# Kernel tuning notes

Hardware: AMD Instinct MI355X
Metric: run time of the kernel (lower is better)

Reference implementation:

```python
import jax, jax.numpy as jnp
import numpy as np

B, K, D, LS, NL = 32, 64, 256, 128, 2


def _xavier(key, shape):
    # torch xavier_uniform for Linear weight [out, in]
    fan_out, fan_in = shape[-2], shape[-1]
    lim = float(np.sqrt(6.0 / (fan_in + fan_out)))
    return jax.random.uniform(key, shape, jnp.float32, -lim, lim)


def setup_inputs():
    key = jax.random.key(0)
    ks = jax.random.split(key, 32)
    inp = {
        "X": jax.random.normal(ks[0], (B, K, D), jnp.float32),
        # per-layer stacked params [NL, ...]
        "k_w": _xavier(ks[1], (NL, D, D)),
        "q_w": _xavier(ks[2], (NL, D, D)),
        "rv_w1": _xavier(ks[3], (NL, D, 2 * D)),
        "rv_b1": jnp.zeros((NL, D), jnp.float32),
        "rv_w2": _xavier(ks[4], (NL, D, D)),
        "rv_b2": jnp.zeros((NL, D), jnp.float32),
        "ln_g": jnp.ones((NL, D), jnp.float32),
        "ln_b": jnp.zeros((NL, D), jnp.float32),
        "mlp_w1": _xavier(ks[5], (NL, D, D)),
        "mlp_b1": jnp.zeros((NL, D), jnp.float32),
        "mlp_w2": _xavier(ks[6], (NL, D, D)),
        "mlp_b2": jnp.zeros((NL, D), jnp.float32),
        "proj_w": _xavier(ks[7], (LS, D)),
        "proj_b": jnp.zeros((LS,), jnp.float32),
        "mu_w": _xavier(ks[8], (LS, LS)),
        "mu_b": jnp.zeros((LS,), jnp.float32),
        "sp_w": _xavier(ks[9], (LS, LS)),
        "sp_b": jnp.zeros((LS,), jnp.float32),
    }
    return inp


def _gelu(x):
    return jax.nn.gelu(x, approximate=False)


def _layernorm(x, g, b, eps=1e-5):
    m = jnp.mean(x, axis=-1, keepdims=True)
    v = jnp.mean((x - m) ** 2, axis=-1, keepdims=True)
    return (x - m) / jnp.sqrt(v + eps) * g + b


def _block(x, kw, qw, rw1, rb1, rw2, rb2, lg, lb, mw1, mb1, mw2, mb2):
    scale = D ** (-0.5)
    x_orig = x
    # pairwise difference r[b,i,j,:] = x[b,i]-x[b,j]
    r = x[:, :, None, :] - x[:, None, :, :]                      # [B,K,K,D]
    xi = jnp.broadcast_to(x[:, :, None, :], (B, K, K, D))
    cat = jnp.concatenate([xi, r], axis=-1)                      # [B,K,K,2D]
    v = _gelu(jnp.einsum('bijc,dc->bijd', cat, rw1) + rb1)
    v = jnp.einsum('bijd,ed->bije', v, rw2) + rb2                # [B,K,K,D]
    k = jnp.einsum('bid,ed->bie', x, kw)
    q = jnp.einsum('bid,ed->bie', x, qw) * scale
    attn = jax.nn.softmax(jnp.einsum('bid,bjd->bij', q, k), axis=2)
    agg = jnp.einsum('bij,bijd->bid', attn, v)
    h = _layernorm(x_orig + agg, lg, lb)
    h = jnp.einsum('bid,ed->bie', _gelu(jnp.einsum('bid,ed->bie', h, mw1) + mb1), mw2) + mb2
    return x_orig + h


def reference(X, k_w, q_w, rv_w1, rv_b1, rv_w2, rv_b2, ln_g, ln_b,
              mlp_w1, mlp_b1, mlp_w2, mlp_b2, proj_w, proj_b,
              mu_w, mu_b, sp_w, sp_b):
    x = X
    for i in range(NL):
        x = _block(x, k_w[i], q_w[i], rv_w1[i], rv_b1[i], rv_w2[i], rv_b2[i],
                   ln_g[i], ln_b[i], mlp_w1[i], mlp_b1[i], mlp_w2[i], mlp_b2[i])
    s = jnp.sum(x, axis=1)                                        # [B,D]
    h = _gelu(s @ proj_w.T + proj_b)                              # [B,LS]
    mu = h @ mu_w.T + mu_b
    scale = jax.nn.softplus(h @ sp_w.T + sp_b)
    return (mu, scale)
```

## Files before the change

### kernel.cpp

```cpp
#include <hip/hip_runtime.h>
#include <hip/hip_bf16.h>


using bf16 = __hip_bfloat16;
typedef short bf16x8 __attribute__((ext_vector_type(8)));
typedef float f32x4 __attribute__((ext_vector_type(4)));

__device__ __forceinline__ float bfu(unsigned short u) { return __uint_as_float(((unsigned)u) << 16); }

__device__ __forceinline__ unsigned short bfr(float v) {
  unsigned u = __float_as_uint(v);
  u += 0x7FFFu + ((u >> 16) & 1u);
  return (unsigned short)(u >> 16);
}

__device__ __forceinline__ float gelu_e(float x) {
  return 0.5f * x * (1.0f + erff(x * 0.7071067811865475f));
}

__device__ __forceinline__ float load_f(const void* p, int i, int fl) {
  if (fl) return bfu(((const unsigned short*)p)[i]);
  return ((const float*)p)[i];
}

__device__ __forceinline__ int block_detect(const void* X) {
  __shared__ int bad_s;
  if (threadIdx.x == 0) bad_s = 0;
  __syncthreads();
  if (threadIdx.x < 256) {
    const float v = bfu(((const unsigned short*)X)[threadIdx.x]);
    if (!(fabsf(v) < 1e6f)) atomicOr(&bad_s, 1);
  }
  __syncthreads();
  return bad_s ? 0 : 1;
}

__device__ __forceinline__ void stage_split4(unsigned short (&aF)[2][4096], int row, int d0, float4 v) {
  ushort4 h, lo;
  h.x = bfr(v.x); h.y = bfr(v.y); h.z = bfr(v.z); h.w = bfr(v.w);
  lo.x = bfr(v.x - bfu(h.x)); lo.y = bfr(v.y - bfu(h.y));
  lo.z = bfr(v.z - bfu(h.z)); lo.w = bfr(v.w - bfu(h.w));
  const int kt = d0 >> 5, lane = row | (((d0 >> 3) & 3) << 4), j = d0 & 7;
  *(ushort4*)&aF[0][kt*512 + lane*8 + j] = h;
  *(ushort4*)&aF[1][kt*512 + lane*8 + j] = lo;
}

__global__ __launch_bounds__(256) void prep_kernel(
    const void* __restrict__ X, const void* __restrict__ kw, const void* __restrict__ qw,
    const void* __restrict__ rw1, const void* __restrict__ rw2, const void* __restrict__ mw1,
    const void* __restrict__ mw2, const void* __restrict__ pw, const void* __restrict__ muw,
    const void* __restrict__ spw,
    const void* __restrict__ rb1, const void* __restrict__ rb2, const void* __restrict__ lng,
    const void* __restrict__ lnb, const void* __restrict__ mb1, const void* __restrict__ mb2,
    const void* __restrict__ pb, const void* __restrict__ mub, const void* __restrict__ spb,
    unsigned short* __restrict__ wfb, unsigned short* __restrict__ w3b,
    float* __restrict__ wh, float* __restrict__ bc)
{
  __shared__ __align__(16) char psm[65536];
  const int fl = block_detect(X);
  const int t = threadIdx.x;
  int blk = blockIdx.x;

  if (blk < 16) {
    unsigned short* ls = (unsigned short*)psm;
    unsigned* lsu = (unsigned*)psm;
    const int l = blk >> 3, kt = blk & 7;
    if (fl) {
      #pragma unroll
      for (int s = 0; s < 4; ++s) {
        const unsigned* sp = (const unsigned*)((s == 0) ? kw : (s == 1) ? qw : rw1);
        const int rstr = (s < 2) ? 128 : 256;
        const int coff = ((s == 3) ? 128 : 0) + kt*16;
        for (int i = t; i < 4096; i += 256) {
          const int e = i >> 4, d2 = i & 15;
          lsu[s*4096 + i] = sp[(l*256 + e)*rstr + coff + d2];
        }
      }
    } else {
      #pragma unroll
      for (int s = 0; s < 4; ++s) {
        const float* sp = (const float*)((s == 0) ? kw : (s == 1) ? qw : rw1);
        const int rstr = (s < 2) ? 256 : 512;
        const int coff = ((s == 3) ? 256 : 0) + kt*32;
        for (int i = t; i < 4096; i += 256) {
          const int e = i >> 4, d2 = i & 15;
          const float f0 = sp[(l*256 + e)*rstr + coff + d2*2];
          const float f1 = sp[(l*256 + e)*rstr + coff + d2*2 + 1];
          lsu[s*4096 + i] = (unsigned)bfr(f0) | ((unsigned)bfr(f1) << 16);
        }
      }
    }
    __syncthreads();
    unsigned* outp = (unsigned*)wfb + (l*8 + kt)*16384;
    for (int f2 = t; f2 < 16384; f2 += 256) {
      const int j2 = f2 & 3, lane = (f2 >> 2) & 63, ntg = f2 >> 8;
      const int seg = ntg >> 4;
      const int e = (ntg & 15)*16 + (lane & 15);
      const int dl = ((lane >> 4) & 3)*8 + j2*2;
      unsigned short r0 = ls[seg*8192 + e*32 + dl];
      unsigned short r1 = ls[seg*8192 + e*32 + dl + 1];
      if (seg == 1) { r0 = bfr(bfu(r0)*0.0625f); r1 = bfr(bfu(r1)*0.0625f); }
      else if (seg == 2) {
        const unsigned short w0 = ls[3*8192 + e*32 + dl];
        const unsigned short w1 = ls[3*8192 + e*32 + dl + 1];
        r0 = bfr(bfu(r0) + bfu(w0)); r1 = bfr(bfu(r1) + bfu(w1));
      }
      outp[f2] = (unsigned)r0 | ((unsigned)r1 << 16);
    }
    return;
// ... 34 lines not shown
  if (blk < 24) {
    float* lsf = (float*)psm;
    if (blk < 8) {
      const int l0 = blk*16;
      if (fl) {
        const unsigned* sp = (const unsigned*)pw;
        for (int i = t; i < 2048; i += 256) {
          const int ll = i >> 7, d2 = i & 127;
          const unsigned u = sp[(l0 + ll)*128 + d2];
          lsf[ll*256 + d2*2]     = __uint_as_float(u << 16);
          lsf[ll*256 + d2*2 + 1] = __uint_as_float(u & 0xffff0000u);
        }
      } else {
        const float* sp = (const float*)pw;
        for (int i = t; i < 4096; i += 256) {
          const int ll = i >> 8, d = i & 255;
          lsf[ll*256 + d] = sp[(l0 + ll)*256 + d];
        }
      }
      __syncthreads();
      for (int i = t; i < 4096; i += 256) {
        const int d = i >> 4, ll = i & 15;
        wh[d*128 + l0 + ll] = lsf[ll*256 + d];
      }
    } else {
      const int grp2 = blk - 8;
      const int isSp = grp2 >> 3;
      const int l0 = (grp2 & 7)*16;
      const void* src = isSp ? spw : muw;
      const int off = isSp ? 49152 : 32768;
      if (fl) {
        const unsigned* sp = (const unsigned*)src;
        for (int i = t; i < 1024; i += 256) {
          const int ll = i >> 6, c2 = i & 63;
          const unsigned u = sp[(l0 + ll)*64 + c2];
          lsf[ll*128 + c2*2]     = __uint_as_float(u << 16);
          lsf[ll*128 + c2*2 + 1] = __uint_as_float(u & 0xffff0000u);
        }
      } else {
        const float* sp = (const float*)src;
        for (int i = t; i < 2048; i += 256) {
          const int ll = i >> 7, c = i & 127;
          lsf[ll*128 + c] = sp[(l0 + ll)*128 + c];
        }
      }
      __syncthreads();
      for (int i = t; i < 2048; i += 256) {
        const int c = i >> 4, ll = i & 15;
        wh[off + c*128 + l0 + ll] = lsf[ll*128 + c];
      }
    }
    return;
  }
  for (int i = t; i < 3456; i += 256) {
    const void* src; int off;
    if (i < 512)       { src = rb1; off = i; }
    else if (i < 1024) { src = rb2; off = i - 512; }
    else if (i < 1536) { src = lng; off = i - 1024; }
    else if (i < 2048) { src = lnb; off = i - 1536; }
    else if (i < 2560) { src = mb1; off = i - 2048; }
    else if (i < 3072) { src = mb2; off = i - 2560; }
    else if (i < 3200) { src = pb;  off = i - 3072; }
    else if (i < 3328) { src = mub; off = i - 3200; }
    else               { src = spb; off = i - 3328; }
    bc[i] = load_f(src, off, fl);
  }
}

template<bool SPLIT, int NTG>
__device__ __forceinline__ void k1_body(
    const unsigned short (&aF)[2][4096],
    const unsigned short* __restrict__ wfb, const float* __restrict__ bc,
    float* __restrict__ kq, float* __restrict__ Pf, unsigned* __restrict__ Qpk,
    int l, int row0, int ntg0, int t)
{
  const int w = t >> 6, l64 = t & 63;
  const int col = l64 & 15, quad = l64 >> 4;
  f32x4 acc[NTG];
  #pragma unroll
  for (int i = 0; i < NTG; ++i) acc[i] = (f32x4){0.f, 0.f, 0.f, 0.f};
  for (int kt = 0; kt < 8; ++kt) {
    const bf16x8 ah = *(const bf16x8*)&aF[0][kt*512 + l64*8];
    bf16x8 al;
    if (SPLIT) al = *(const bf16x8*)&aF[1][kt*512 + l64*8];
    #pragma unroll
    for (int i = 0; i < NTG; ++i) {
      const int ntg = ntg0 + w*NTG + i;
      const bf16x8 b = *(const bf16x8*)&wfb[((l*8 + kt)*64 + ntg)*512 + l64*8];
      acc[i] = __builtin_amdgcn_mfma_f32_16x16x32_bf16(ah, b, acc[i], 0, 0, 0);
      if (SPLIT) acc[i] = __builtin_amdgcn_mfma_f32_16x16x32_bf16(al, b, acc[i], 0, 0, 0);
    }
  }
  #pragma unroll
  for (int i = 0; i < NTG; ++i) {
    const int ntg = ntg0 + w*NTG + i;
    if (ntg < 32) {
      const int n = ntg*16 + col;
      #pragma unroll
      for (int r = 0; r < 4; ++r)
        kq[(size_t)(row0 + quad*4 + r)*512 + n] = acc[i][r];
    } else if (ntg < 48) {
      const int c = (ntg - 32)*16 + col;
      const float bias = bc[l*256 + c];
      #pragma unroll
      for (int r = 0; r < 4; ++r)
        Pf[(size_t)(row0 + quad*4 + r)*256 + c] = acc[i][r] + bias;
    } else {
      #pragma unroll
      for (int r = 0; r < 4; ++r) {
        const float v = acc[i][r];
        const float pv = __shfl_xor(v, 1, 64);
        if (!(col & 1)) {
          const unsigned uu = (unsigned)bfr(v) | ((unsigned)bfr(pv) << 16);
          Qpk[(size_t)(row0 + quad*4 + r)*128 + (ntg - 48)*8 + (col >> 1)] = uu;
        }
      }
    }
  }
}

__global__ __launch_bounds__(256) void k1l0(
    const void* __restrict__ X, const unsigned short* __restrict__ wfb,
    const float* __restrict__ bc, float* __restrict__ kq, float* __restrict__ Pf,
    unsigned* __restrict__ Qpk)
{
  const int fl = block_detect(X);
  __shared__ __align__(16) unsigned short aF[2][4096];
  const int t = threadIdx.x;
  const int mb = (int)blockIdx.x >> 2, nb4 = (int)blockIdx.x & 3;
  const int row0 = mb * 16, ntg0 = nb4 * 16;
  if (fl) {
    for (int i = t; i < 512; i += 256) {
      const int row = i >> 5, d0 = (i & 31) * 8;
      const uint4 u = *(const uint4*)((const unsigned*)X + (size_t)(row0 + row)*128 + (i & 31)*4);
      const int kt = d0 >> 5, lane = row | (((d0 >> 3) & 3) << 4);
      *(uint4*)&aF[0][kt*512 + lane*8] = u;
    }
  } else {
    for (int i = t; i < 1024; i += 256) {
      const int row = i >> 6, d0 = (i & 63) * 4;
      stage_split4(aF, row, d0, *(const float4*)((const float*)X + (size_t)(row0 + row)*256 + d0));
    }
  }
  __syncthreads();
  if (fl) k1_body<false, 4>(aF, wfb, bc, kq, Pf, Qpk, 0, row0, ntg0, t);
  else    k1_body<true,  4>(aF, wfb, bc, kq, Pf, Qpk, 0, row0, ntg0, t);
}

__global__ __launch_bounds__(256) void k23_attn(
    const float* __restrict__ kq, const float* __restrict__ Pf,
    const unsigned* __restrict__ Qpk, float* __restrict__ g)
{
  __shared__ float qs[2][256];
  __shared__ float scp[2][64];
  __shared__ float als[2][64];
  const int t = threadIdx.x;
  const int b = (int)blockIdx.x >> 5, ip = (int)blockIdx.x & 31;
  const int base = b << 6, i0 = ip * 2;
  for (int i = t; i < 512; i += 256)
    qs[i >> 8][i & 255] = kq[(size_t)(base + i0 + (i >> 8))*512 + 256 + (i & 255)];
  __syncthreads();
  {
    const int w = t >> 6, lane = t & 63;
    const int jl = lane & 15, part = lane >> 4;
    const int j = w*16 + jl;
    const float* krow = kq + (size_t)(base + j)*512 + part*64;
    const float* q0p = &qs[0][part*64];
    const float* q1p = &qs[1][part*64];
    float s0 = 0.f, s1 = 0.f;
    for (int dd = 0; dd < 64; dd += 4) {
      const float4 kv = *(const float4*)&krow[dd];
      const float4 q0 = *(const float4*)&q0p[dd];
      const float4 q1 = *(const float4*)&q1p[dd];
      s0 = fmaf(kv.x, q0.x, s0); s0 = fmaf(kv.y, q0.y, s0);
      s0 = fmaf(kv.z, q0.z, s0); s0 = fmaf(kv.w, q0.w, s0);
      s1 = fmaf(kv.x, q1.x, s1); s1 = fmaf(kv.y, q1.y, s1);
      s1 = fmaf(kv.z, q1.z, s1); s1 = fmaf(kv.w, q1.w, s1);
    }
    s0 += __shfl_xor(s0, 16, 64); s0 += __shfl_xor(s0, 32, 64);
    s1 += __shfl_xor(s1, 16, 64); s1 += __shfl_xor(s1, 32, 64);
    if (part == 0) { scp[0][j] = s0; scp[1][j] = s1; }
  }
  __syncthreads();
  if (t < 128) {
    const int row = t >> 6, j = t & 63;
    float s = scp[row][j];
    float m = s;
    #pragma unroll
    for (int off = 32; off; off >>= 1) m = fmaxf(m, __shfl_xor(m, off, 64));
    const float e = __expf(s - m);
    float ss = e;
    #pragma unroll
    for (int off = 32; off; off >>= 1) ss += __shfl_xor(ss, off, 64);
    als[row][j] = e / ss;
  }
  __syncthreads();
  const int rg = t >> 7, cp = t & 127;
  const int r = base + i0 + rg;
  const float2 P = *(const float2*)&Pf[(size_t)r*256 + cp*2];
  const float A0 = -1.702f * P.x, A1 = -1.702f * P.y;
  const float* ap = &als[rg][0];
  const unsigned* qp = Qpk + (size_t)base*128 + cp;
  float acc0 = 0.f, acc1 = 0.f;
  #pragma unroll 8
  for (int j = 0; j < 64; ++j) {
    const unsigned u = qp[j*128];
    const float wgt = ap[j];
    const float q0 = __uint_as_float(u << 16);
    const float q1 = __uint_as_float(u & 0xffff0000u);
    const float s0 = __builtin_amdgcn_rcpf(1.f + __expf(fmaf(1.702f, q0, A0)));
    const float s1 = __builtin_amdgcn_rcpf(1.f + __expf(fmaf(1.702f, q1, A1)));
    acc0 = fmaf(wgt * (P.x - q0), s0, acc0);
    acc1 = fmaf(wgt * (P.y - q1), s1, acc1);
  }
  *(float2*)&g[(size_t)r*256 + cp*2] = make_float2(acc0, acc1);
}

__device__ __forceinline__ void k4_gemm8(
    f32x4 acc[2], const unsigned short (&aF)[2][4096],
    const unsigned short* __restrict__ wg, int w, int l64)
{
  acc[0] = (f32x4){0.f, 0.f, 0.f, 0.f};
  acc[1] = (f32x4){0.f, 0.f, 0.f, 0.f};
  for (int kt = 0; kt < 8; ++kt) {
    const bf16x8 ah = *(const bf16x8*)&aF[0][kt*512 + l64*8];
    const bf16x8 al = *(const bf16x8*)&aF[1][kt*512 + l64*8];
    #pragma unroll
    for (int nt = 0; nt < 2; ++nt) {
      const bf16x8 b = *(const bf16x8*)&wg[((kt*16 + (w*2 + nt))*64 + l64)*8];
      acc[nt] = __builtin_amdgcn_mfma_f32_16x16x32_bf16(ah, b, acc[nt], 0, 0, 0);
      acc[nt] = __builtin_amdgcn_mfma_f32_16x16x32_bf16(al, b, acc[nt], 0, 0, 0);
    }
  }
}

template<bool ADAPT, bool TAIL, int NR>
__device__ __forceinline__ void k4_core(
    const float* __restrict__ g, const void* __restrict__ xin, int fl,
    float* __restrict__ xout, const unsigned short* __restrict__ wg,
    const float* __restrict__ bc, int l, int row0, int t, bool writeX,
    unsigned short (&aF)[2][4096], float* bufB, float (&mv)[16][2])
{
  const int w = t >> 6, l64 = t & 63;
  const int col = l64 & 15, quad = l64 >> 4;
  const float* rb2c = bc + 512  + l*256;
  const float* lngc = bc + 1024 + l*256;
  const float* lnbc = bc + 1536 + l*256;
  const float* mb1c = bc + 2048 + l*256;
  const float* mb2c = bc + 2560 + l*256;

  for (int i = t; i < NR*64; i += 512) {
    const int row = i >> 6, d0 = (i & 63) * 4;
    stage_split4(aF, row, d0, *(const float4*)&g[(size_t)(row0 + row)*256 + d0]);
  }
  if (ADAPT && fl) {
    for (int c = t; c < NR*128; c += 512) {
      const int row = c >> 7, dp = c & 127;
      const unsigned u = ((const unsigned*)xin)[(size_t)(row0 + row)*128 + dp];
      bufB[row*260 + dp*2]     = __uint_as_float(u << 16);
      bufB[row*260 + dp*2 + 1] = __uint_as_float(u & 0xffff0000u);
    }
  } else {
    for (int c = t; c < NR*64; c += 512) {
      const int row = c >> 6, d0 = (c & 63) * 4;
      *(float4*)&bufB[row*260 + d0] = *(const float4*)((const float*)xin + (size_t)(row0 + row)*256 + d0);
    }
  }
  __syncthreads();
  float xtr[2][4];
  #pragma unroll
  for (int nt = 0; nt < 2; ++nt) {
    const int cn = (w*2 + nt)*16 + col;
    #pragma unroll
    for (int r = 0; r < 4; ++r) xtr[nt][r] = bufB[(quad*4 + r)*260 + cn];
  }
  __syncthreads();

  f32x4 acc[2];
  k4_gemm8(acc, aF, wg, w, l64);
  #pragma unroll
  for (int nt = 0; nt < 2; ++nt) {
    const int cn = (w*2 + nt)*16 + col;
    #pragma unroll
    for (int r = 0; r < 4; ++r)
      bufB[(quad*4 + r)*260 + cn] = acc[nt][r] + rb2c[cn] + xtr[nt][r];
  }
  __syncthreads();
  {
    const int row = t >> 5, part = t & 31;
    if (row < NR) {
      float s = 0.f, s2 = 0.f;
      #pragma unroll
      for (int kk = 0; kk < 8; ++kk) {
        const float v = bufB[row*260 + part + kk*32];
        s += v; s2 = fmaf(v, v, s2);
      }
      #pragma unroll
      for (int off = 16; off; off >>= 1) {
        s  += __shfl_xor(s, off, 32);
        s2 += __shfl_xor(s2, off, 32);
      }
      if (part == 0) {
        const float mu = s * (1.f/256.f);
        mv[row][0] = mu;
        mv[row][1] = rsqrtf(fmaf(-mu, mu, s2 * (1.f/256.f)) + 1e-5f);
      }
// ... 5 lines not shown
    float4 v = *(const float4*)&bufB[row*260 + d0];
    const float m = mv[row][0], iv = mv[row][1];
    v.x = (v.x - m)*iv*lngc[d0]   + lnbc[d0];
    v.y = (v.y - m)*iv*lngc[d0+1] + lnbc[d0+1];
    v.z = (v.z - m)*iv*lngc[d0+2] + lnbc[d0+2];
    v.w = (v.w - m)*iv*lngc[d0+3] + lnbc[d0+3];
    stage_split4(aF, row, d0, v);
  }
  __syncthreads();
  k4_gemm8(acc, aF, wg + 65536, w, l64);
  #pragma unroll
  for (int nt = 0; nt < 2; ++nt) {
    const int cn = (w*2 + nt)*16 + col;
    #pragma unroll
    for (int r = 0; r < 4; ++r)
      if (quad*4 + r < NR)
        bufB[(quad*4 + r)*260 + cn] = gelu_e(acc[nt][r] + mb1c[cn]);
  }
  __syncthreads();
  for (int i = t; i < NR*64; i += 512) {
    const int row = i >> 6, d0 = (i & 63) * 4;
    stage_split4(aF, row, d0, *(const float4*)&bufB[row*260 + d0]);
  }
  __syncthreads();
  k4_gemm8(acc, aF, wg + 2*65536, w, l64);
  if (TAIL) {
    #pragma unroll
    for (int nt = 0; nt < 2; ++nt) {
      const int cn = (w*2 + nt)*16 + col;
      #pragma unroll
      for (int r = 0; r < 4; ++r)
        bufB[(quad*4 + r)*260 + cn] = acc[nt][r] + mb2c[cn] + xtr[nt][r];
    }
    __syncthreads();
    for (int i = t; i < NR*64; i += 512) {
      const int row = i >> 6, d0 = (i & 63) * 4;
      const float4 v = *(const float4*)&bufB[row*260 + d0];
      if (writeX) *(float4*)&xout[(size_t)(row0 + row)*256 + d0] = v;
      stage_split4(aF, row, d0, v);
    }
    __syncthreads();
  } else {
    #pragma unroll
    for (int nt = 0; nt < 2; ++nt) {
      const int cn = (w*2 + nt)*16 + col;
      #pragma unroll
      for (int r = 0; r < 4; ++r)
        if (quad*4 + r < NR)
          xout[(size_t)(row0 + quad*4 + r)*256 + cn] = acc[nt][r] + mb2c[cn] + xtr[nt][r];
    }
  }
}

__global__ __launch_bounds__(512) void k41_mix_kq(
    const float* __restrict__ g, const unsigned short* __restrict__ w3b,
    const unsigned short* __restrict__ wfb, const float* __restrict__ bc,
    const void* __restrict__ X, float* __restrict__ x,
    float* __restrict__ kq, float* __restrict__ Pf, unsigned* __restrict__ Qpk)
{
  const int fl = block_detect(X);
  __shared__ __align__(16) unsigned short aF[2][4096];
  __shared__ float bufB[16*260];
  __shared__ float mv[16][2];
  const int t = threadIdx.x;
  const int rb = (int)blockIdx.x >> 1, parity = (int)blockIdx.x & 1;
  const int row0 = rb * 16;
  k4_core<true, true, 16>(g, X, fl, x, w3b, bc, 0, row0, t, parity == 0, aF, bufB, mv);
  k1_body<true, 4>(aF, wfb, bc, kq, Pf, Qpk, 1, row0, parity*32, t);
}

__global__ __launch_bounds__(512) void k4_fin(
    const float* __restrict__ g, const unsigned short* __restrict__ w3b,
    const float* __restrict__ bc, float* __restrict__ x)
{
  __shared__ __align__(16) unsigned short aF[2][4096];
  __shared__ float bufB[16*260];
  __shared__ float mv[16][2];
  const int t = threadIdx.x;
  const int row0 = blockIdx.x * 8;
  k4_core<false, false, 8>(g, x, 0, x, w3b + 3*65536, bc, 1, row0, t, true, aF, bufB, mv);
}

__global__ __launch_bounds__(256) void k5_head(
    const float* __restrict__ x, const float* __restrict__ wh,
    const float* __restrict__ bc, const void* __restrict__ X,
    void* __restrict__ out)
{
  const int fl = block_detect(X);
  __shared__ float ss[256];
  __shared__ float hh[128];
  const int b = blockIdx.x, t = threadIdx.x;
  float s = 0.f;
  for (int i = 0; i < 64; ++i) s += x[(size_t)((b << 6) + i)*256 + t];
  ss[t] = s;
  __syncthreads();
  if (t < 128) {
    float acc = bc[3072 + t];
    const float* projT = wh;
    for (int d = 0; d < 256; ++d) acc = fmaf(ss[d], projT[d*128 + t], acc);
    hh[t] = gelu_e(acc);
  }
  __syncthreads();
  float v; int oidx;
  if (t < 128) {
    float acc = bc[3200 + t];
    const float* muT = wh + 32768;
    for (int c = 0; c < 128; ++c) acc = fmaf(hh[c], muT[c*128 + t], acc);
    v = acc; oidx = b*128 + t;
  } else {
    const int u = t - 128;
    float acc = bc[3328 + u];
    const float* spT = wh + 49152;
    for (int c = 0; c < 128; ++c) acc = fmaf(hh[c], spT[c*128 + u], acc);
    v = (acc > 20.f) ? acc : log1pf(__expf(acc));
    oidx = 4096 + b*128 + u;
  }
  if (fl) ((bf16*)out)[oidx] = __float2bfloat16(v);
  else    ((float*)out)[oidx] = v;
}

extern "C" void kernel_launch(void* const* d_in, const int* in_sizes, int n_in,
                              void* d_out, int out_size, void* d_ws, size_t ws_size,
                              hipStream_t stream)
{
  (void)in_sizes; (void)n_in; (void)out_size; (void)ws_size;
  float* ws    = (float*)d_ws;
  float* x     = ws + 16;
  float* kq    = x + 524288;
  float* Pf    = kq + 1048576;
  unsigned* Qpk = (unsigned*)(Pf + 524288);
  float* g     = (float*)(Qpk + 262144);
  unsigned short* wfb = (unsigned short*)(g + 524288);
  unsigned short* w3b = wfb + 524288;
  float* wh    = (float*)(w3b + 393216);
  float* bc    = wh + 65536;

  prep_kernel<<<dim3(89), dim3(256), 0, stream>>>(
      d_in[0], d_in[1], d_in[2], d_in[3], d_in[5], d_in[9], d_in[11],
      d_in[13], d_in[15], d_in[17],
      d_in[4], d_in[6], d_in[7], d_in[8], d_in[10], d_in[12],
      d_in[14], d_in[16], d_in[18],
      wfb, w3b, wh, bc);
  k1l0<<<dim3(512), dim3(256), 0, stream>>>(d_in[0], wfb, bc, kq, Pf, Qpk);
  k23_attn<<<dim3(1024), dim3(256), 0, stream>>>(kq, Pf, Qpk, g);
  k41_mix_kq<<<dim3(256), dim3(512), 0, stream>>>(g, w3b, wfb, bc, d_in[0], x, kq, Pf, Qpk);
  k23_attn<<<dim3(1024), dim3(256), 0, stream>>>(kq, Pf, Qpk, g);
  k4_fin<<<dim3(256), dim3(512), 0, stream>>>(g, w3b, bc, x);
  k5_head<<<dim3(32), dim3(256), 0, stream>>>(x, wh, bc, d_in[0], (void*)d_out);
}
```

Before: 206.5 us.

## Fuse all layer kernels into one cooperative persistent kernel with grid syncs

Replaces six separate kernel launches (k1, two attention passes, the mix/kq kernel, the final k4 and the head) with one cooperative kernel of 256 blocks that runs each stage in turn, separated by grid-wide barriers. The attention phase now processes four units per block across two iterations and two halves, and the k4 mix stage is split from the layer-1 kq projection with an extra grid sync. The aim is to remove launch overhead and inter-kernel gaps. In exchange, occupancy is limited to a single resident wave of blocks, shared memory per block grows, and each stage now pays for grid.sync barriers.

After: 428.5 us. 2.07x slower.

```diff
diff --git a/kernel.cpp b/kernel.cpp
--- a/kernel.cpp
+++ b/kernel.cpp
@@ -1,5 +1,8 @@
 #include <hip/hip_runtime.h>
 #include <hip/hip_bf16.h>
+#include <hip/hip_cooperative_groups.h>
+
+namespace cg = cooperative_groups;
 
 
 using bf16 = __hip_bfloat16;
@@ -262,101 +265,78 @@
   }
 }
 
-__global__ __launch_bounds__(256) void k1l0(
-    const void* __restrict__ X, const unsigned short* __restrict__ wfb,
-    const float* __restrict__ bc, float* __restrict__ kq, float* __restrict__ Pf,
-    unsigned* __restrict__ Qpk)
-{
-  const int fl = block_detect(X);
-  __shared__ __align__(16) unsigned short aF[2][4096];
-  const int t = threadIdx.x;
-  const int mb = (int)blockIdx.x >> 2, nb4 = (int)blockIdx.x & 3;
-  const int row0 = mb * 16, ntg0 = nb4 * 16;
-  if (fl) {
-    for (int i = t; i < 512; i += 256) {
-      const int row = i >> 5, d0 = (i & 31) * 8;
-      const uint4 u = *(const uint4*)((const unsigned*)X + (size_t)(row0 + row)*128 + (i & 31)*4);
-      const int kt = d0 >> 5, lane = row | (((d0 >> 3) & 3) << 4);
-      *(uint4*)&aF[0][kt*512 + lane*8] = u;
-    }
-  } else {
-    for (int i = t; i < 1024; i += 256) {
-      const int row = i >> 6, d0 = (i & 63) * 4;
-      stage_split4(aF, row, d0, *(const float4*)((const float*)X + (size_t)(row0 + row)*256 + d0));
-    }
-  }
-  __syncthreads();
-  if (fl) k1_body<false, 4>(aF, wfb, bc, kq, Pf, Qpk, 0, row0, ntg0, t);
-  else    k1_body<true,  4>(aF, wfb, bc, kq, Pf, Qpk, 0, row0, ntg0, t);
-}
-
-__global__ __launch_bounds__(256) void k23_attn(
+__device__ __forceinline__ void k23_phase(
     const float* __restrict__ kq, const float* __restrict__ Pf,
-    const unsigned* __restrict__ Qpk, float* __restrict__ g)
-{
-  __shared__ float qs[2][256];
-  __shared__ float scp[2][64];
-  __shared__ float als[2][64];
-  const int t = threadIdx.x;
-  const int b = (int)blockIdx.x >> 5, ip = (int)blockIdx.x & 31;
-  const int base = b << 6, i0 = ip * 2;
-  for (int i = t; i < 512; i += 256)
-    qs[i >> 8][i & 255] = kq[(size_t)(base + i0 + (i >> 8))*512 + 256 + (i & 255)];
-  __syncthreads();
-  {
-    const int w = t >> 6, lane = t & 63;
-    const int jl = lane & 15, part = lane >> 4;
-    const int j = w*16 + jl;
-    const float* krow = kq + (size_t)(base + j)*512 + part*64;
-    const float* q0p = &qs[0][part*64];
-    const float* q1p = &qs[1][part*64];
-    float s0 = 0.f, s1 = 0.f;
-    for (int dd = 0; dd < 64; dd += 4) {
-      const float4 kv = *(const float4*)&krow[dd];
-      const float4 q0 = *(const float4*)&q0p[dd];
-      const float4 q1 = *(const float4*)&q1p[dd];
-      s0 = fmaf(kv.x, q0.x, s0); s0 = fmaf(kv.y, q0.y, s0);
-      s0 = fmaf(kv.z, q0.z, s0); s0 = fmaf(kv.w, q0.w, s0);
-      s1 = fmaf(kv.x, q1.x, s1); s1 = fmaf(kv.y, q1.y, s1);
-      s1 = fmaf(kv.z, q1.z, s1); s1 = fmaf(kv.w, q1.w, s1);
-    }
-    s0 += __shfl_xor(s0, 16, 64); s0 += __shfl_xor(s0, 32, 64);
-    s1 += __shfl_xor(s1, 16, 64); s1 += __shfl_xor(s1, 32, 64);
-    if (part == 0) { scp[0][j] = s0; scp[1][j] = s1; }
-  }
-  __syncthreads();
-  if (t < 128) {
-    const int row = t >> 6, j = t & 63;
-    float s = scp[row][j];
-    float m = s;
-    #pragma unroll
-    for (int off = 32; off; off >>= 1) m = fmaxf(m, __shfl_xor(m, off, 64));
-    const float e = __expf(s - m);
-    float ss = e;
-    #pragma unroll
-    for (int off = 32; off; off >>= 1) ss += __shfl_xor(ss, off, 64);
-    als[row][j] = e / ss;
-  }
-  __syncthreads();
-  const int rg = t >> 7, cp = t & 127;
-  const int r = base + i0 + rg;
-  const float2 P = *(const float2*)&Pf[(size_t)r*256 + cp*2];
-  const float A0 = -1.702f * P.x, A1 = -1.702f * P.y;
-  const float* ap = &als[rg][0];
-  const unsigned* qp = Qpk + (size_t)base*128 + cp;
-  float acc0 = 0.f, acc1 = 0.f;
-  #pragma unroll 8
-  for (int j = 0; j < 64; ++j) {
-    const unsigned u = qp[j*128];
-    const float wgt = ap[j];
-    const float q0 = __uint_as_float(u << 16);
-    const float q1 = __uint_as_float(u & 0xffff0000u);
-    const float s0 = __builtin_amdgcn_rcpf(1.f + __expf(fmaf(1.702f, q0, A0)));
-    const float s1 = __builtin_amdgcn_rcpf(1.f + __expf(fmaf(1.702f, q1, A1)));
-    acc0 = fmaf(wgt * (P.x - q0), s0, acc0);
-    acc1 = fmaf(wgt * (P.y - q1), s1, acc1);
-  }
-  *(float2*)&g[(size_t)r*256 + cp*2] = make_float2(acc0, acc1);
+    const unsigned* __restrict__ Qpk, float* __restrict__ g,
+    int bid, int t,
+    float (&qs)[2][2][256], float (&scp)[2][2][64], float (&als)[2][2][64])
+{
+  const int half = t >> 8, tt = t & 255;
+  for (int it = 0; it < 2; ++it) {
+    __syncthreads();
+    const int unit = (bid << 2) | (half << 1) | it;
+    const int b = unit >> 5, ip = unit & 31;
+    const int base = b << 6, i0 = ip * 2;
+    for (int i = tt; i < 512; i += 256)
+      qs[half][i >> 8][i & 255] = kq[(size_t)(base + i0 + (i >> 8))*512 + 256 + (i & 255)];
+    __syncthreads();
+    {
+      const int w = tt >> 6, lane = t & 63;
+      const int jl = lane & 15, part = lane >> 4;
+      const int j = w*16 + jl;
+      const float* krow = kq + (size_t)(base + j)*512 + part*64;
+      const float* q0p = &qs[half][0][part*64];
+      const float* q1p = &qs[half][1][part*64];
+      float s0 = 0.f, s1 = 0.f;
+      for (int dd = 0; dd < 64; dd += 4) {
+        const float4 kv = *(const float4*)&krow[dd];
+        const float4 q0 = *(const float4*)&q0p[dd];
+        const float4 q1 = *(const float4*)&q1p[dd];
+        s0 = fmaf(kv.x, q0.x, s0); s0 = fmaf(kv.y, q0.y, s0);
+        s0 = fmaf(kv.z, q0.z, s0); s0 = fmaf(kv.w, q0.w, s0);
+        s1 = fmaf(kv.x, q1.x, s1); s1 = fmaf(kv.y, q1.y, s1);
+        s1 = fmaf(kv.z, q1.z, s1); s1 = fmaf(kv.w, q1.w, s1);
+      }
+      s0 += __shfl_xor(s0, 16, 64); s0 += __shfl_xor(s0, 32, 64);
+      s1 += __shfl_xor(s1, 16, 64); s1 += __shfl_xor(s1, 32, 64);
+      if (part == 0) { scp[half][0][j] = s0; scp[half][1][j] = s1; }
+    }
+    __syncthreads();
+    if (tt < 128) {
+      const int row = tt >> 6, j = t & 63;
+      float s = scp[half][row][j];
+      float m = s;
+      #pragma unroll
+      for (int off = 32; off; off >>= 1) m = fmaxf(m, __shfl_xor(m, off, 64));
+      const float e = __expf(s - m);
+      float ss = e;
+      #pragma unroll
+      for (int off = 32; off; off >>= 1) ss += __shfl_xor(ss, off, 64);
+      als[half][row][j] = e / ss;
+    }
+    __syncthreads();
+    {
+      const int rg = tt >> 7, cp = tt & 127;
+      const int r = base + i0 + rg;
+      const float2 P = *(const float2*)&Pf[(size_t)r*256 + cp*2];
+      const float A0 = -1.702f * P.x, A1 = -1.702f * P.y;
+      const float* ap = &als[half][rg][0];
+      const unsigned* qp = Qpk + (size_t)base*128 + cp;
+      float acc0 = 0.f, acc1 = 0.f;
+      #pragma unroll 8
+      for (int j = 0; j < 64; ++j) {
+        const unsigned u = qp[j*128];
+        const float wgt = ap[j];
+        const float q0 = __uint_as_float(u << 16);
+        const float q1 = __uint_as_float(u & 0xffff0000u);
+        const float s0 = __builtin_amdgcn_rcpf(1.f + __expf(fmaf(1.702f, q0, A0)));
+        const float s1 = __builtin_amdgcn_rcpf(1.f + __expf(fmaf(1.702f, q1, A1)));
+        acc0 = fmaf(wgt * (P.x - q0), s0, acc0);
+        acc1 = fmaf(wgt * (P.y - q1), s1, acc1);
+      }
+      *(float2*)&g[(size_t)r*256 + cp*2] = make_float2(acc0, acc1);
+    }
+  }
 }
 
 __device__ __forceinline__ void k4_gemm8(
@@ -506,71 +486,114 @@
   }
 }
 
-__global__ __launch_bounds__(512) void k41_mix_kq(
-    const float* __restrict__ g, const unsigned short* __restrict__ w3b,
-    const unsigned short* __restrict__ wfb, const float* __restrict__ bc,
-    const void* __restrict__ X, float* __restrict__ x,
-    float* __restrict__ kq, float* __restrict__ Pf, unsigned* __restrict__ Qpk)
-{
+__device__ __forceinline__ void k5_phase(
+    const float* __restrict__ x, const float* __restrict__ wh,
+    const float* __restrict__ bc, int fl, void* __restrict__ out,
+    int b, int t, float (&ss2)[2][256], float (&hh)[128])
+{
+  const int half = t >> 8, tt = t & 255;
+  {
+    float s = 0.f;
+    const float* xp = x + (size_t)((b << 6) + half*32)*256 + tt;
+    #pragma unroll 8
+    for (int i = 0; i < 32; ++i) s += xp[(size_t)i*256];
+    ss2[half][tt] = s;
+  }
+  __syncthreads();
+  if (t < 128) {
+    float acc = bc[3072 + t];
+    const float* projT = wh;
+    for (int d = 0; d < 256; ++d) acc = fmaf(ss2[0][d] + ss2[1][d], projT[d*128 + t], acc);
+    hh[t] = gelu_e(acc);
+  }
+  __syncthreads();
+  if (t < 256) {
+    float v; int oidx;
+    if (t < 128) {
+      float acc = bc[3200 + t];
+      const float* muT = wh + 32768;
+      for (int c = 0; c < 128; ++c) acc = fmaf(hh[c], muT[c*128 + t], acc);
+      v = acc; oidx = b*128 + t;
+    } else {
+      const int u2 = t - 128;
+      float acc = bc[3328 + u2];
+      const float* spT = wh + 49152;
+      for (int c = 0; c < 128; ++c) acc = fmaf(hh[c], spT[c*128 + u2], acc);
+      v = (acc > 20.f) ? acc : log1pf(__expf(acc));
+      oidx = 4096 + b*128 + u2;
+    }
+    if (fl) ((bf16*)out)[oidx] = __float2bfloat16(v);
+    else    ((float*)out)[oidx] = v;
+  }
+}
+
+__global__ __launch_bounds__(512) void mega(
+    const void* __restrict__ X, const unsigned short* __restrict__ wfb,
+    const unsigned short* __restrict__ w3b, const float* __restrict__ wh,
+    const float* __restrict__ bc, float* __restrict__ x,
+    float* __restrict__ kq, float* __restrict__ Pf, unsigned* __restrict__ Qpk,
+    float* __restrict__ g, void* __restrict__ out)
+{
+  cg::grid_group grid = cg::this_grid();
   const int fl = block_detect(X);
   __shared__ __align__(16) unsigned short aF[2][4096];
   __shared__ float bufB[16*260];
   __shared__ float mv[16][2];
+  __shared__ float qs[2][2][256];
+  __shared__ float scp[2][2][64];
+  __shared__ float als[2][2][64];
+  __shared__ float ss2[2][256];
+  __shared__ float hh[128];
   const int t = threadIdx.x;
-  const int rb = (int)blockIdx.x >> 1, parity = (int)blockIdx.x & 1;
-  const int row0 = rb * 16;
-  k4_core<true, true, 16>(g, X, fl, x, w3b, bc, 0, row0, t, parity == 0, aF, bufB, mv);
-  k1_body<true, 4>(aF, wfb, bc, kq, Pf, Qpk, 1, row0, parity*32, t);
-}
-
-__global__ __launch_bounds__(512) void k4_fin(
-    const float* __restrict__ g, const unsigned short* __restrict__ w3b,
-    const float* __restrict__ bc, float* __restrict__ x)
-{
-  __shared__ __align__(16) unsigned short aF[2][4096];
-  __shared__ float bufB[16*260];
-  __shared__ float mv[16][2];
-  const int t = threadIdx.x;
-  const int row0 = blockIdx.x * 8;
-  k4_core<false, false, 8>(g, x, 0, x, w3b + 3*65536, bc, 1, row0, t, true, aF, bufB, mv);
-}
-
-__global__ __launch_bounds__(256) void k5_head(
-    const float* __restrict__ x, const float* __restrict__ wh,
-    const float* __restrict__ bc, const void* __restrict__ X,
-    void* __restrict__ out)
-{
-  const int fl = block_detect(X);
-  __shared__ float ss[256];
-  __shared__ float hh[128];
-  const int b = blockIdx.x, t = threadIdx.x;
-  float s = 0.f;
-  for (int i = 0; i < 64; ++i) s += x[(size_t)((b << 6) + i)*256 + t];
-  ss[t] = s;
-  __syncthreads();
-  if (t < 128) {
-    float acc = bc[3072 + t];
-    const float* projT = wh;
-    for (int d = 0; d < 256; ++d) acc = fmaf(ss[d], projT[d*128 + t], acc);
-    hh[t] = gelu_e(acc);
-  }
-  __syncthreads();
-  float v; int oidx;
-  if (t < 128) {
-    float acc = bc[3200 + t];
-    const float* muT = wh + 32768;
-    for (int c = 0; c < 128; ++c) acc = fmaf(hh[c], muT[c*128 + t], acc);
-    v = acc; oidx = b*128 + t;
-  } else {
-    const int u = t - 128;
-    float acc = bc[3328 + u];
-    const float* spT = wh + 49152;
-    for (int c = 0; c < 128; ++c) acc = fmaf(hh[c], spT[c*128 + u], acc);
-    v = (acc > 20.f) ? acc : log1pf(__expf(acc));
-    oidx = 4096 + b*128 + u;
-  }
-  if (fl) ((bf16*)out)[oidx] = __float2bfloat16(v);
-  else    ((float*)out)[oidx] = v;
+  const int bid = (int)blockIdx.x;
+
+  {
+    const int row0 = (bid >> 1) * 16, ntg0 = (bid & 1) * 32;
+    if (fl) {
+      const int i = t;
+      if (i < 512) {
+        const int row = i >> 5;
+        const uint4 u = *(const uint4*)((const unsigned*)X + (size_t)(row0 + row)*128 + (i & 31)*4);
+        const int d0 = (i & 31) * 8;
+        const int kt = d0 >> 5, lane = row | (((d0 >> 3) & 3) << 4);
+        *(uint4*)&aF[0][kt*512 + lane*8] = u;
+      }
+    } else {
+      for (int i = t; i < 1024; i += 512) {
+        const int row = i >> 6, d0 = (i & 63) * 4;
+        stage_split4(aF, row, d0, *(const float4*)((const float*)X + (size_t)(row0 + row)*256 + d0));
+      }
+    }
+    __syncthreads();
+    if (fl) k1_body<false, 4>(aF, wfb, bc, kq, Pf, Qpk, 0, row0, ntg0, t);
+    else    k1_body<true,  4>(aF, wfb, bc, kq, Pf, Qpk, 0, row0, ntg0, t);
+  }
+  grid.sync();
+
+  k23_phase(kq, Pf, Qpk, g, bid, t, qs, scp, als);
+  grid.sync();
+
+  k4_core<true, false, 8>(g, X, fl, x, w3b, bc, 0, bid*8, t, true, aF, bufB, mv);
+  grid.sync();
+
+  {
+    const int row0 = (bid >> 1) * 16, ntg0 = (bid & 1) * 32;
+    for (int i = t; i < 1024; i += 512) {
+      const int row = i >> 6, d0 = (i & 63) * 4;
+      stage_split4(aF, row, d0, *(const float4*)&x[(size_t)(row0 + row)*256 + d0]);
+    }
+    __syncthreads();
+    k1_body<true, 4>(aF, wfb, bc, kq, Pf, Qpk, 1, row0, ntg0, t);
+  }
+  grid.sync();
+
+  k23_phase(kq, Pf, Qpk, g, bid, t, qs, scp, als);
+  grid.sync();
+
+  k4_core<false, false, 8>(g, x, 0, x, w3b + 3*65536, bc, 1, bid*8, t, true, aF, bufB, mv);
+  grid.sync();
+
+  if (bid < 32) k5_phase(x, wh, bc, fl, out, bid, t, ss2, hh);
 }
 
 extern "C" void kernel_launch(void* const* d_in, const int* in_sizes, int n_in,
@@ -595,10 +618,11 @@
       d_in[4], d_in[6], d_in[7], d_in[8], d_in[10], d_in[12],
       d_in[14], d_in[16], d_in[18],
       wfb, w3b, wh, bc);
-  k1l0<<<dim3(512), dim3(256), 0, stream>>>(d_in[0], wfb, bc, kq, Pf, Qpk);
-  k23_attn<<<dim3(1024), dim3(256), 0, stream>>>(kq, Pf, Qpk, g);
-  k41_mix_kq<<<dim3(256), dim3(512), 0, stream>>>(g, w3b, wfb, bc, d_in[0], x, kq, Pf, Qpk);
-  k23_attn<<<dim3(1024), dim3(256), 0, stream>>>(kq, Pf, Qpk, g);
-  k4_fin<<<dim3(256), dim3(512), 0, stream>>>(g, w3b, bc, x);
-  k5_head<<<dim3(32), dim3(256), 0, stream>>>(x, wh, bc, d_in[0], (void*)d_out);
-}
+
+  const void* Xp = d_in[0];
+  void* outp = d_out;
+  void* args[] = { (void*)&Xp, (void*)&wfb, (void*)&w3b, (void*)&wh, (void*)&bc,
+                   (void*)&x, (void*)&kq, (void*)&Pf, (void*)&Qpk, (void*)&g,
+                   (void*)&outp };
+  hipLaunchCooperativeKernel((const void*)mega, dim3(256), dim3(512), args, 0, stream);
+}
```

## Fuse final MLP and head kernels using a global atomic completion counter

Applied to the files above, without the earlier changes.

Merges the last block-MLP kernel with the pooling/projection head by having every block increment a device-scope atomic counter after finishing its rows. The first 32 blocks then spin until all 256 blocks are done and compute the head themselves. The head work is also spread over 512 threads with split reductions. This removes one kernel launch and its gap, but depends on all 256 blocks being co-resident or at least the waiting blocks not starving the others, plus a counter reset in the prep kernel.

After: 265.5 us. +28.5%, slower.

```diff
diff --git a/kernel.cpp b/kernel.cpp
--- a/kernel.cpp
+++ b/kernel.cpp
@@ -54,7 +54,7 @@
     const void* __restrict__ lnb, const void* __restrict__ mb1, const void* __restrict__ mb2,
     const void* __restrict__ pb, const void* __restrict__ mub, const void* __restrict__ spb,
     unsigned short* __restrict__ wfb, unsigned short* __restrict__ w3b,
-    float* __restrict__ wh, float* __restrict__ bc)
+    float* __restrict__ wh, float* __restrict__ bc, unsigned* __restrict__ cnt)
 {
   __shared__ __align__(16) char psm[65536];
   const int fl = block_detect(X);
@@ -195,6 +195,7 @@
     }
     return;
   }
+  if (t == 0) *cnt = 0u;
   for (int i = t; i < 3456; i += 256) {
     const void* src; int off;
     if (i < 512)       { src = rb1; off = i; }
@@ -523,54 +524,80 @@
   k1_body<true, 4>(aF, wfb, bc, kq, Pf, Qpk, 1, row0, parity*32, t);
 }
 
-__global__ __launch_bounds__(512) void k4_fin(
+__global__ __launch_bounds__(512) void k4fin5(
     const float* __restrict__ g, const unsigned short* __restrict__ w3b,
-    const float* __restrict__ bc, float* __restrict__ x)
-{
+    const float* __restrict__ bc, float* __restrict__ x,
+    const float* __restrict__ wh, const void* __restrict__ X,
+    void* __restrict__ out, unsigned* __restrict__ cnt)
+{
+  const int fl = block_detect(X);
   __shared__ __align__(16) unsigned short aF[2][4096];
   __shared__ float bufB[16*260];
   __shared__ float mv[16][2];
   const int t = threadIdx.x;
-  const int row0 = blockIdx.x * 8;
+  const int bid = (int)blockIdx.x;
+  const int row0 = bid * 8;
   k4_core<false, false, 8>(g, x, 0, x, w3b + 3*65536, bc, 1, row0, t, true, aF, bufB, mv);
-}
-
-__global__ __launch_bounds__(256) void k5_head(
-    const float* __restrict__ x, const float* __restrict__ wh,
-    const float* __restrict__ bc, const void* __restrict__ X,
-    void* __restrict__ out)
-{
-  const int fl = block_detect(X);
-  __shared__ float ss[256];
-  __shared__ float hh[128];
-  const int b = blockIdx.x, t = threadIdx.x;
-  float s = 0.f;
-  for (int i = 0; i < 64; ++i) s += x[(size_t)((b << 6) + i)*256 + t];
-  ss[t] = s;
-  __syncthreads();
-  if (t < 128) {
-    float acc = bc[3072 + t];
-    const float* projT = wh;
-    for (int d = 0; d < 256; ++d) acc = fmaf(ss[d], projT[d*128 + t], acc);
-    hh[t] = gelu_e(acc);
-  }
-  __syncthreads();
-  float v; int oidx;
-  if (t < 128) {
-    float acc = bc[3200 + t];
-    const float* muT = wh + 32768;
-    for (int c = 0; c < 128; ++c) acc = fmaf(hh[c], muT[c*128 + t], acc);
-    v = acc; oidx = b*128 + t;
-  } else {
-    const int u = t - 128;
-    float acc = bc[3328 + u];
-    const float* spT = wh + 49152;
-    for (int c = 0; c < 128; ++c) acc = fmaf(hh[c], spT[c*128 + u], acc);
-    v = (acc > 20.f) ? acc : log1pf(__expf(acc));
-    oidx = 4096 + b*128 + u;
-  }
-  if (fl) ((bf16*)out)[oidx] = __float2bfloat16(v);
-  else    ((float*)out)[oidx] = v;
+
+  __threadfence();
+  __syncthreads();
+  if (t == 0) __hip_atomic_fetch_add(cnt, 1u, __ATOMIC_RELEASE, __HIP_MEMORY_SCOPE_AGENT);
+  if (bid >= 32) return;
+  if (t == 0) {
+    while (__hip_atomic_load(cnt, __ATOMIC_ACQUIRE, __HIP_MEMORY_SCOPE_AGENT) < 256u)
+      __builtin_amdgcn_s_sleep(2);
+  }
+  __syncthreads();
+  __threadfence();
+
+  float* ss2 = bufB;
+  float* hh  = bufB + 512;
+  float* red = bufB + 640;
+  {
+    const int half = t >> 8, tt = t & 255;
+    float s = 0.f;
+    const float* xp = x + (size_t)((bid << 6) + half*32)*256 + tt;
+    #pragma unroll 8
+    for (int i = 0; i < 32; ++i) s += xp[(size_t)i*256];
+    ss2[half*256 + tt] = s;
+  }
+  __syncthreads();
+  if (t < 256) {
+    const int o = t & 127, dh = t >> 7;
+    float acc = 0.f;
+    #pragma unroll 4
+    for (int d = dh*128; d < dh*128 + 128; ++d)
+      acc = fmaf(ss2[d] + ss2[256 + d], wh[d*128 + o], acc);
+    red[t] = acc;
+  }
+  __syncthreads();
+  if (t < 128) hh[t] = gelu_e(red[t] + red[128 + t] + bc[3072 + t]);
+  __syncthreads();
+  {
+    const int grp = t >> 7, o = t & 127;
+    const int isSp = grp >> 1, ch = grp & 1;
+    const float* W = wh + (isSp ? 49152 : 32768);
+    float acc = 0.f;
+    #pragma unroll 4
+    for (int c = ch*64; c < ch*64 + 64; ++c)
+      acc = fmaf(hh[c], W[c*128 + o], acc);
+    red[t] = acc;
+  }
+  __syncthreads();
+  if (t < 256) {
+    const int isSp = t >> 7, o = t & 127;
+    float v; int oidx;
+    if (isSp == 0) {
+      v = red[o] + red[128 + o] + bc[3200 + o];
+      oidx = bid*128 + o;
+    } else {
+      const float a = red[256 + o] + red[384 + o] + bc[3328 + o];
+      v = (a > 20.f) ? a : log1pf(__expf(a));
+      oidx = 4096 + bid*128 + o;
+    }
+    if (fl) ((bf16*)out)[oidx] = __float2bfloat16(v);
+    else    ((float*)out)[oidx] = v;
+  }
 }
 
 extern "C" void kernel_launch(void* const* d_in, const int* in_sizes, int n_in,
@@ -579,6 +606,7 @@
 {
   (void)in_sizes; (void)n_in; (void)out_size; (void)ws_size;
   float* ws    = (float*)d_ws;
+  unsigned* cnt = (unsigned*)ws;
   float* x     = ws + 16;
   float* kq    = x + 524288;
   float* Pf    = kq + 1048576;
@@ -594,11 +622,10 @@
       d_in[13], d_in[15], d_in[17],
       d_in[4], d_in[6], d_in[7], d_in[8], d_in[10], d_in[12],
       d_in[14], d_in[16], d_in[18],
-      wfb, w3b, wh, bc);
+      wfb, w3b, wh, bc, cnt);
   k1l0<<<dim3(512), dim3(256), 0, stream>>>(d_in[0], wfb, bc, kq, Pf, Qpk);
   k23_attn<<<dim3(1024), dim3(256), 0, stream>>>(kq, Pf, Qpk, g);
   k41_mix_kq<<<dim3(256), dim3(512), 0, stream>>>(g, w3b, wfb, bc, d_in[0], x, kq, Pf, Qpk);
   k23_attn<<<dim3(1024), dim3(256), 0, stream>>>(kq, Pf, Qpk, g);
-  k4_fin<<<dim3(256), dim3(512), 0, stream>>>(g, w3b, bc, x);
-  k5_head<<<dim3(32), dim3(256), 0, stream>>>(x, wh, bc, d_in[0], (void*)d_out);
-}
+  k4fin5<<<dim3(256), dim3(512), 0, stream>>>(g, w3b, bc, x, wh, d_in[0], (void*)d_out, cnt);
+}
```

## Fuse attention aggregation into the following mix/kq and final MLP kernels

Applied to the files above, without the earlier changes.

Moves the attention-aggregation kernel into the two following kernels as a prologue that writes the aggregated rows into shared memory instead of global g. Two launches and the global round trip of g go away. Layer 1's kq/P/Q outputs go to separate workspace buffers so a block cannot overwrite data another block is still reading. In exchange, each 512-thread block now computes attention for 16 (or 8) rows with more shared memory, and the two parity blocks per row group duplicate the attention work. Overall parallelism for the attention phase is lower than in the old 1024-block launch.

After: 215.7 us. +4.4%, slower.

```diff
diff --git a/kernel.cpp b/kernel.cpp
--- a/kernel.cpp
+++ b/kernel.cpp
@@ -290,44 +290,45 @@
   else    k1_body<true,  4>(aF, wfb, bc, kq, Pf, Qpk, 0, row0, ntg0, t);
 }
 
-__global__ __launch_bounds__(256) void k23_attn(
+template<int NR>
+__device__ __forceinline__ void attn_phase(
     const float* __restrict__ kq, const float* __restrict__ Pf,
-    const unsigned* __restrict__ Qpk, float* __restrict__ g)
-{
-  __shared__ float qs[2][256];
-  __shared__ float scp[2][64];
-  __shared__ float als[2][64];
-  const int t = threadIdx.x;
-  const int b = (int)blockIdx.x >> 5, ip = (int)blockIdx.x & 31;
-  const int base = b << 6, i0 = ip * 2;
-  for (int i = t; i < 512; i += 256)
-    qs[i >> 8][i & 255] = kq[(size_t)(base + i0 + (i >> 8))*512 + 256 + (i & 255)];
-  __syncthreads();
+    const unsigned* __restrict__ Qpk,
+    int row0, int t, float* qg, float* scp, float* als)
+{
+  const int base = row0 & ~63;
+  for (int i = t; i < NR*64; i += 512) {
+    const int il = i >> 6, d0 = (i & 63)*4;
+    *(float4*)&qg[il*256 + d0] = *(const float4*)&kq[(size_t)(row0 + il)*512 + 256 + d0];
+  }
+  __syncthreads();
+  const int w = t >> 6, lane = t & 63;
   {
-    const int w = t >> 6, lane = t & 63;
     const int jl = lane & 15, part = lane >> 4;
-    const int j = w*16 + jl;
-    const float* krow = kq + (size_t)(base + j)*512 + part*64;
-    const float* q0p = &qs[0][part*64];
-    const float* q1p = &qs[1][part*64];
-    float s0 = 0.f, s1 = 0.f;
-    for (int dd = 0; dd < 64; dd += 4) {
-      const float4 kv = *(const float4*)&krow[dd];
-      const float4 q0 = *(const float4*)&q0p[dd];
-      const float4 q1 = *(const float4*)&q1p[dd];
-      s0 = fmaf(kv.x, q0.x, s0); s0 = fmaf(kv.y, q0.y, s0);
-      s0 = fmaf(kv.z, q0.z, s0); s0 = fmaf(kv.w, q0.w, s0);
-      s1 = fmaf(kv.x, q1.x, s1); s1 = fmaf(kv.y, q1.y, s1);
-      s1 = fmaf(kv.z, q1.z, s1); s1 = fmaf(kv.w, q1.w, s1);
-    }
-    s0 += __shfl_xor(s0, 16, 64); s0 += __shfl_xor(s0, 32, 64);
-    s1 += __shfl_xor(s1, 16, 64); s1 += __shfl_xor(s1, 32, 64);
-    if (part == 0) { scp[0][j] = s0; scp[1][j] = s1; }
-  }
-  __syncthreads();
-  if (t < 128) {
-    const int row = t >> 6, j = t & 63;
-    float s = scp[row][j];
+    const int j = (w & 3)*16 + jl;
+    for (int p = 0; p < NR/4; ++p) {
+      const int i0 = (p*2 + (w >> 2))*2;
+      const float* krow = kq + (size_t)(base + j)*512 + part*64;
+      const float* q0p = &qg[i0*256 + part*64];
+      const float* q1p = &qg[(i0+1)*256 + part*64];
+      float s0 = 0.f, s1 = 0.f;
+      for (int dd = 0; dd < 64; dd += 4) {
+        const float4 kv = *(const float4*)&krow[dd];
+        const float4 q0 = *(const float4*)&q0p[dd];
+        const float4 q1 = *(const float4*)&q1p[dd];
+        s0 = fmaf(kv.x, q0.x, s0); s0 = fmaf(kv.y, q0.y, s0);
+        s0 = fmaf(kv.z, q0.z, s0); s0 = fmaf(kv.w, q0.w, s0);
+        s1 = fmaf(kv.x, q1.x, s1); s1 = fmaf(kv.y, q1.y, s1);
+        s1 = fmaf(kv.z, q1.z, s1); s1 = fmaf(kv.w, q1.w, s1);
+      }
+      s0 += __shfl_xor(s0, 16, 64); s0 += __shfl_xor(s0, 32, 64);
+      s1 += __shfl_xor(s1, 16, 64); s1 += __shfl_xor(s1, 32, 64);
+      if (part == 0) { scp[i0*64 + j] = s0; scp[(i0+1)*64 + j] = s1; }
+    }
+  }
+  __syncthreads();
+  for (int r = w; r < NR; r += 8) {
+    float s = scp[r*64 + lane];
     float m = s;
     #pragma unroll
     for (int off = 32; off; off >>= 1) m = fmaxf(m, __shfl_xor(m, off, 64));
@@ -335,28 +336,42 @@
     float ss = e;
     #pragma unroll
     for (int off = 32; off; off >>= 1) ss += __shfl_xor(ss, off, 64);
-    als[row][j] = e / ss;
-  }
-  __syncthreads();
-  const int rg = t >> 7, cp = t & 127;
-  const int r = base + i0 + rg;
-  const float2 P = *(const float2*)&Pf[(size_t)r*256 + cp*2];
-  const float A0 = -1.702f * P.x, A1 = -1.702f * P.y;
-  const float* ap = &als[rg][0];
-  const unsigned* qp = Qpk + (size_t)base*128 + cp;
-  float acc0 = 0.f, acc1 = 0.f;
-  #pragma unroll 8
-  for (int j = 0; j < 64; ++j) {
-    const unsigned u = qp[j*128];
-    const float wgt = ap[j];
-    const float q0 = __uint_as_float(u << 16);
-    const float q1 = __uint_as_float(u & 0xffff0000u);
-    const float s0 = __builtin_amdgcn_rcpf(1.f + __expf(fmaf(1.702f, q0, A0)));
-    const float s1 = __builtin_amdgcn_rcpf(1.f + __expf(fmaf(1.702f, q1, A1)));
-    acc0 = fmaf(wgt * (P.x - q0), s0, acc0);
-    acc1 = fmaf(wgt * (P.y - q1), s1, acc1);
-  }
-  *(float2*)&g[(size_t)r*256 + cp*2] = make_float2(acc0, acc1);
+    als[r*64 + lane] = e / ss;
+  }
+  __syncthreads();
+  {
+    constexpr int RK = NR/4;
+    const int cp = t & 127, rb4 = t >> 7;
+    float Px[RK], Py[RK], A0[RK], A1[RK], a0[RK], a1[RK];
+    #pragma unroll
+    for (int k = 0; k < RK; ++k) {
+      const float2 P = *(const float2*)&Pf[(size_t)(row0 + rb4*RK + k)*256 + cp*2];
+      Px[k] = P.x; Py[k] = P.y;
+      A0[k] = -1.702f * P.x; A1[k] = -1.702f * P.y;
+      a0[k] = 0.f; a1[k] = 0.f;
+    }
+    const unsigned* qp = Qpk + (size_t)base*128 + cp;
+    #pragma unroll 4
+    for (int j = 0; j < 64; ++j) {
+      const unsigned u = qp[j*128];
+      const float q0 = __uint_as_float(u << 16);
+      const float q1 = __uint_as_float(u & 0xffff0000u);
+      #pragma unroll
+      for (int k = 0; k < RK; ++k) {
+        const float wgt = als[(rb4*RK + k)*64 + j];
+        const float s0 = __builtin_amdgcn_rcpf(1.f + __expf(fmaf(1.702f, q0, A0[k])));
+        const float s1 = __builtin_amdgcn_rcpf(1.f + __expf(fmaf(1.702f, q1, A1[k])));
+        a0[k] = fmaf(wgt * (Px[k] - q0), s0, a0[k]);
+        a1[k] = fmaf(wgt * (Py[k] - q1), s1, a1[k]);
+      }
+    }
+    #pragma unroll
+    for (int k = 0; k < RK; ++k) {
+      qg[(rb4*RK + k)*256 + cp*2]     = a0[k];
+      qg[(rb4*RK + k)*256 + cp*2 + 1] = a1[k];
+    }
+  }
+  __syncthreads();
 }
 
 __device__ __forceinline__ void k4_gemm8(
@@ -379,7 +394,7 @@
 
 template<bool ADAPT, bool TAIL, int NR>
 __device__ __forceinline__ void k4_core(
-    const float* __restrict__ g, const void* __restrict__ xin, int fl,
+    const float* gl, const void* __restrict__ xin, int fl,
     float* __restrict__ xout, const unsigned short* __restrict__ wg,
     const float* __restrict__ bc, int l, int row0, int t, bool writeX,
     unsigned short (&aF)[2][4096], float* bufB, float (&mv)[16][2])
@@ -394,7 +409,7 @@
 
   for (int i = t; i < NR*64; i += 512) {
     const int row = i >> 6, d0 = (i & 63) * 4;
-    stage_split4(aF, row, d0, *(const float4*)&g[(size_t)(row0 + row)*256 + d0]);
+    stage_split4(aF, row, d0, *(const float4*)&gl[row*256 + d0]);
   }
   if (ADAPT && fl) {
     for (int c = t; c < NR*128; c += 512) {
@@ -506,33 +521,43 @@
   }
 }
 
-__global__ __launch_bounds__(512) void k41_mix_kq(
-    const float* __restrict__ g, const unsigned short* __restrict__ w3b,
-    const unsigned short* __restrict__ wfb, const float* __restrict__ bc,
-    const void* __restrict__ X, float* __restrict__ x,
-    float* __restrict__ kq, float* __restrict__ Pf, unsigned* __restrict__ Qpk)
+__global__ __launch_bounds__(512) void kA_attn_mix_kq(
+    const unsigned short* __restrict__ w3b, const unsigned short* __restrict__ wfb,
+    const float* __restrict__ bc, const void* __restrict__ X, float* __restrict__ x,
+    const float* __restrict__ kq, const float* __restrict__ Pf,
+    const unsigned* __restrict__ Qpk,
+    float* __restrict__ kq1, float* __restrict__ Pf1, unsigned* __restrict__ Qpk1)
 {
   const int fl = block_detect(X);
   __shared__ __align__(16) unsigned short aF[2][4096];
-  __shared__ float bufB[16*260];
+  __shared__ __align__(16) float bufB[16*260];
   __shared__ float mv[16][2];
+  __shared__ __align__(16) float qg[16*256];
+  __shared__ float scp[16*64];
+  __shared__ float als[16*64];
   const int t = threadIdx.x;
   const int rb = (int)blockIdx.x >> 1, parity = (int)blockIdx.x & 1;
   const int row0 = rb * 16;
-  k4_core<true, true, 16>(g, X, fl, x, w3b, bc, 0, row0, t, parity == 0, aF, bufB, mv);
-  k1_body<true, 4>(aF, wfb, bc, kq, Pf, Qpk, 1, row0, parity*32, t);
-}
-
-__global__ __launch_bounds__(512) void k4_fin(
-    const float* __restrict__ g, const unsigned short* __restrict__ w3b,
-    const float* __restrict__ bc, float* __restrict__ x)
+  attn_phase<16>(kq, Pf, Qpk, row0, t, qg, scp, als);
+  k4_core<true, true, 16>(qg, X, fl, x, w3b, bc, 0, row0, t, parity == 0, aF, bufB, mv);
+  k1_body<true, 4>(aF, wfb, bc, kq1, Pf1, Qpk1, 1, row0, parity*32, t);
+}
+
+__global__ __launch_bounds__(512) void kB_attn_fin(
+    const unsigned short* __restrict__ w3b, const float* __restrict__ bc,
+    float* __restrict__ x, const float* __restrict__ kq1,
+    const float* __restrict__ Pf1, const unsigned* __restrict__ Qpk1)
 {
   __shared__ __align__(16) unsigned short aF[2][4096];
-  __shared__ float bufB[16*260];
+  __shared__ __align__(16) float bufB[16*260];
   __shared__ float mv[16][2];
+  __shared__ __align__(16) float qg[8*256];
+  __shared__ float scp[8*64];
+  __shared__ float als[8*64];
   const int t = threadIdx.x;
-  const int row0 = blockIdx.x * 8;
-  k4_core<false, false, 8>(g, x, 0, x, w3b + 3*65536, bc, 1, row0, t, true, aF, bufB, mv);
+  const int row0 = (int)blockIdx.x * 8;
+  attn_phase<8>(kq1, Pf1, Qpk1, row0, t, qg, scp, als);
+  k4_core<false, false, 8>(qg, x, 0, x, w3b + 3*65536, bc, 1, row0, t, true, aF, bufB, mv);
 }
 
 __global__ __launch_bounds__(256) void k5_head(
@@ -588,6 +613,9 @@
   unsigned short* w3b = wfb + 524288;
   float* wh    = (float*)(w3b + 393216);
   float* bc    = wh + 65536;
+  float* kq1   = bc + 4096;
+  float* Pf1   = kq1 + 1048576;
+  unsigned* Qpk1 = (unsigned*)(Pf1 + 524288);
 
   prep_kernel<<<dim3(89), dim3(256), 0, stream>>>(
       d_in[0], d_in[1], d_in[2], d_in[3], d_in[5], d_in[9], d_in[11],
@@ -596,9 +624,8 @@
       d_in[14], d_in[16], d_in[18],
       wfb, w3b, wh, bc);
   k1l0<<<dim3(512), dim3(256), 0, stream>>>(d_in[0], wfb, bc, kq, Pf, Qpk);
-  k23_attn<<<dim3(1024), dim3(256), 0, stream>>>(kq, Pf, Qpk, g);
-  k41_mix_kq<<<dim3(256), dim3(512), 0, stream>>>(g, w3b, wfb, bc, d_in[0], x, kq, Pf, Qpk);
-  k23_attn<<<dim3(1024), dim3(256), 0, stream>>>(kq, Pf, Qpk, g);
-  k4_fin<<<dim3(256), dim3(512), 0, stream>>>(g, w3b, bc, x);
+  kA_attn_mix_kq<<<dim3(256), dim3(512), 0, stream>>>(
+      w3b, wfb, bc, d_in[0], x, kq, Pf, Qpk, kq1, Pf1, Qpk1);
+  kB_attn_fin<<<dim3(256), dim3(512), 0, stream>>>(w3b, bc, x, kq1, Pf1, Qpk1);
   k5_head<<<dim3(32), dim3(256), 0, stream>>>(x, wh, bc, d_in[0], (void*)d_out);
 }
```
